# Optimization experiments

Measured on AMD Instinct MI355X. Metric: run time of the kernel, lower is better.

The kernel has to match this reference:

```python
import jax, jax.numpy as jnp
import numpy as np

TEMPERATURE = 0.5
EPS = 1e-12  # matches torch F.normalize eps


def _l2_normalize(x):
    norm = jnp.linalg.norm(x, axis=-1, keepdims=True)
    return x / jnp.maximum(norm, EPS)


def setup_inputs() -> dict:
    key = jax.random.key(0)
    k1, k2, k3 = jax.random.split(key, 3)
    N, D = 16384, 128
    self_predictions = jax.random.normal(k1, (N, D), dtype=jnp.float32)
    pos_predictions = jax.random.normal(k2, (N, D), dtype=jnp.float32)
    labels1 = jax.random.randint(k3, (N,), 0, 100, dtype=jnp.int64)
    return {
        "self_predictions": self_predictions,
        "pos_predictions": pos_predictions,
        "labels1": labels1,
    }


def reference(self_predictions, pos_predictions, labels1):
    N = labels1.shape[0]
    a = _l2_normalize(self_predictions)  # [N, D]
    b = _l2_normalize(pos_predictions)   # [N, D]
    # cosine similarity of already-normalized rows == dot product (GEMM form)
    sim = jnp.einsum("nd,md->nm", a, b)  # [N, N]
    neg_mask = (labels1[:, None] != labels1[None, :]).astype(sim.dtype)  # 1 - mask
    neg = jnp.exp(-sim / TEMPERATURE) * neg_mask
    return neg.sum() / (N * (N - 1))
```

## Files before the change

### kernel.cpp

```cpp
#include <hip/hip_runtime.h>

typedef unsigned char u8;
typedef unsigned short u16;
typedef float f32x4 __attribute__((ext_vector_type(4)));
typedef int i32x4 __attribute__((ext_vector_type(4)));
typedef int i32x8 __attribute__((ext_vector_type(8)));

#define NROWS 16384
#define DIM 128

#define NEG2LOG2E -2.8853900817779268f
#define SCALE ((float)(1.0 / (16384.0 * 16383.0)))

#define SCALE1 0x7F7F7F7F

#define KMAX 320

__global__ __launch_bounds__(256) void norm_kernel(
    const float* __restrict__ a, const float* __restrict__ b,
    u8* __restrict__ aO, u8* __restrict__ bO)
{
    int tid  = threadIdx.x;
    int lane = tid & 63;
    int w    = tid >> 6;
    int half = lane >> 5;
    int l32  = lane & 31;
    long row = (long)blockIdx.x * 8 + w * 2 + half;

    const float4 va = ((const float4*)(a + row * DIM))[l32];
    float sa = va.x * va.x + va.y * va.y + va.z * va.z + va.w * va.w;
    #pragma unroll
    for (int off = 16; off; off >>= 1) sa += __shfl_xor(sa, off, 64);
    float inva = 1.0f / fmaxf(sqrtf(sa), 1e-12f);
    int pa = __builtin_amdgcn_cvt_pk_fp8_f32(va.x * inva, va.y * inva, 0, false);
    pa = __builtin_amdgcn_cvt_pk_fp8_f32(va.z * inva, va.w * inva, pa, true);
    ((int*)(aO + row * DIM))[l32] = pa;

    const float4 vb = ((const float4*)(b + row * DIM))[l32];
    float sb = vb.x * vb.x + vb.y * vb.y + vb.z * vb.z + vb.w * vb.w;
    #pragma unroll
    for (int off = 16; off; off >>= 1) sb += __shfl_xor(sb, off, 64);
    float invb = NEG2LOG2E / fmaxf(sqrtf(sb), 1e-12f);
    int pb = __builtin_amdgcn_cvt_pk_fp8_f32(vb.x * invb, vb.y * invb, 0, false);
    pb = __builtin_amdgcn_cvt_pk_fp8_f32(vb.z * invb, vb.w * invb, pb, true);
    ((int*)(bO + row * DIM))[l32] = pb;
}

__global__ __launch_bounds__(256, 3) void gemm_kernel(
    const u8* __restrict__ A, const u8* __restrict__ B,
    const int* __restrict__ labels,
    float* __restrict__ partials, float* __restrict__ corrP)
{
    __shared__ u8 sA[16384];
    __shared__ u8 sB[2][16384];

    int tid  = threadIdx.x;
    int lane = tid & 63;
    int w    = tid >> 6;
    int mrow = lane & 15;
    int q    = lane >> 4;

    if (blockIdx.x == 32) {
        if (blockIdx.y >= 100) return;
        int l = blockIdx.y;
        int* sIdx = (int*)sA;
        __shared__ int sCnt;
        __shared__ float red[4];
        if (tid == 0) sCnt = 0;
        __syncthreads();

        for (int i = tid; i < NROWS; i += 256)
            if (labels[i] == l) {
                int p = atomicAdd(&sCnt, 1);
                if (p < KMAX) sIdx[p] = i;
            }
        __syncthreads();

        int k = sCnt < KMAX ? sCnt : KMAX;
        int nt = (k + 15) >> 4;
        int ntk = nt << 4;
        for (int r = k + tid; r < ntk; r += 256) sIdx[r] = sIdx[0];
        __syncthreads();

        float s = 0.0f;
        for (int tp = w; tp < nt * nt; tp += 4) {
            int ti = tp / nt, tj = tp - ti * nt;
            int ri = sIdx[ti * 16 + mrow];
            int rj = sIdx[tj * 16 + mrow];
            const u8* pa = A + (size_t)ri * DIM + q * 32;
            const u8* pb = B + (size_t)rj * DIM + q * 32;
            i32x8 aF, bF;
            *((i32x4*)&aF)     = *(const i32x4*)pa;
            *((i32x4*)&aF + 1) = *(const i32x4*)(pa + 16);
            *((i32x4*)&bF)     = *(const i32x4*)pb;
            *((i32x4*)&bF + 1) = *(const i32x4*)(pb + 16);
            f32x4 acc = (f32x4){0.f, 0.f, 0.f, 0.f};
            acc = __builtin_amdgcn_mfma_scale_f32_16x16x128_f8f6f4(
                aF, bF, acc, 0, 0, 0, SCALE1, 0, SCALE1);
            int i0 = ti * 16 + q * 4;
            int j  = tj * 16 + mrow;
            #pragma unroll
            for (int r = 0; r < 4; r++) {
                float e = __builtin_amdgcn_exp2f(acc[r]);
                s += ((i0 + r) < k && j < k) ? e : 0.0f;
            }
        }

        #pragma unroll
        for (int off = 32; off; off >>= 1) s += __shfl_xor(s, off, 64);
        if (lane == 0) red[w] = s;
        __syncthreads();
        if (tid == 0)
            corrP[l] = (red[0] + red[1] + red[2] + red[3]) * SCALE;
        return;
    }

    int wr = w >> 1;
    int wc = w & 1;

    int rowBase = blockIdx.y * 128;
    int colBase = blockIdx.x * 512;

    int m0 = tid >> 3;
    int p0 = tid & 7;
    int srcOff = m0 * 128 + ((p0 ^ (m0 & 7)) << 4);
    int ldsOff = (tid - lane) * 16;

    const u8* gA = A + (size_t)rowBase * DIM + srcOff;
    const u8* gB = B + (size_t)colBase * DIM + srcOff;

    {
        const u8* gpA = gA;
        const u8* gpB = gB;
        u8* lpA = &sA[ldsOff];
        u8* lpB = &sB[0][ldsOff];
        #pragma unroll
        for (int it = 0; it < 4; it++) {
            __builtin_amdgcn_global_load_lds(
                (const __attribute__((address_space(1))) void*)gpA,
                (__attribute__((address_space(3))) void*)lpA, 16, 0, 0);
            __builtin_amdgcn_global_load_lds(
                (const __attribute__((address_space(1))) void*)gpB,
                (__attribute__((address_space(3))) void*)lpB, 16, 0, 0);
            gpA += 4096; gpB += 4096; lpA += 4096; lpB += 4096;
        }
    }

    int aOff[4], bOff[4];
    #pragma unroll
    for (int mi = 0; mi < 4; mi++) {
        int m = wr * 64 + mi * 16 + mrow;
        aOff[mi] = m * 128 + (((q << 1) ^ (m & 7)) << 4);
        int n = wc * 64 + mi * 16 + mrow;
        bOff[mi] = n * 128 + (((q << 1) ^ (n & 7)) << 4);
    }

    __syncthreads();

    i32x8 a8[4];
    #pragma unroll
    for (int mi = 0; mi < 4; mi++) {
        *((i32x4*)&a8[mi])     = *(const i32x4*)(sA + aOff[mi]);
        *((i32x4*)&a8[mi] + 1) = *(const i32x4*)(sA + (aOff[mi] ^ 16));
    }

    float s = 0.0f;

    #pragma unroll
    for (int jt = 0; jt < 4; jt++) {
        if (jt < 3) {
            const u8* gp = gB + (jt + 1) * (128 * DIM);
            u8* lp = &sB[(jt + 1) & 1][ldsOff];
            #pragma unroll
            for (int it = 0; it < 4; it++) {
                __builtin_amdgcn_global_load_lds(
                    (const __attribute__((address_space(1))) void*)gp,
                    (__attribute__((address_space(3))) void*)lp, 16, 0, 0);
                gp += 4096; lp += 4096;
            }
        }

        const u8* sb = sB[jt & 1];
        i32x8 b8[4];
        #pragma unroll
        for (int ni = 0; ni < 4; ni++) {
            *((i32x4*)&b8[ni])     = *(const i32x4*)(sb + bOff[ni]);
            *((i32x4*)&b8[ni] + 1) = *(const i32x4*)(sb + (bOff[ni] ^ 16));
        }

        f32x4 acc[4][4];
        #pragma unroll
        for (int mi = 0; mi < 4; mi++)
            #pragma unroll
            for (int ni = 0; ni < 4; ni++)
                acc[mi][ni] = (f32x4){0.f, 0.f, 0.f, 0.f};

        #pragma unroll
        for (int mi = 0; mi < 4; mi++)
            #pragma unroll
            for (int ni = 0; ni < 4; ni++)
                acc[mi][ni] = __builtin_amdgcn_mfma_scale_f32_16x16x128_f8f6f4(
                    a8[mi], b8[ni], acc[mi][ni], 0, 0, 0, SCALE1, 0, SCALE1);

        float s0 = 0.0f, s1 = 0.0f;
        #pragma unroll
        for (int mi = 0; mi < 4; mi++)
            #pragma unroll
            for (int ni = 0; ni < 4; ni++)
                #pragma unroll
                for (int r = 0; r < 4; r++) {
                    float e = __builtin_amdgcn_exp2f(acc[mi][ni][r]);
                    if (r & 1) s1 += e; else s0 += e;
                }
        s += s0 + s1;

        __syncthreads();
    }

    #pragma unroll
    for (int off = 32; off; off >>= 1) s += __shfl_xor(s, off, 64);

    float* red = (float*)sA;
    if (lane == 0) red[w] = s;
    __syncthreads();
    if (tid == 0) {
        float t = (red[0] + red[1]) + (red[2] + red[3]);
        partials[blockIdx.y * 32 + blockIdx.x] = t * SCALE;
    }
}

__global__ __launch_bounds__(256) void reduce_kernel(
    const float* __restrict__ gP, const float* __restrict__ cP,
    float* __restrict__ out)
{
    int tid = threadIdx.x;
    const float4* p4 = (const float4*)gP;
    float s = 0.0f;
    #pragma unroll 4
    for (int i = tid; i < 1024; i += 256) {
        float4 v = p4[i];
        s += (v.x + v.y) + (v.z + v.w);
    }
    if (tid < 100) s -= cP[tid];
    #pragma unroll
    for (int off = 32; off; off >>= 1) s += __shfl_xor(s, off, 64);
    __shared__ float red[4];
    if ((tid & 63) == 0) red[tid >> 6] = s;
    __syncthreads();
    if (tid == 0) out[0] = (red[0] + red[1]) + (red[2] + red[3]);
}

extern "C" void kernel_launch(void* const* d_in, const int* in_sizes, int n_in,
                              void* d_out, int out_size, void* d_ws, size_t ws_size,
                              hipStream_t stream) {
    const float* self_p = (const float*)d_in[0];
    const float* pos_p  = (const float*)d_in[1];
    const int*   labels = (const int*)d_in[2];
    float* out = (float*)d_out;

    u8* aB = (u8*)d_ws;
    u8* bB = aB + (size_t)NROWS * DIM;
    float* gemmP = (float*)(bB + (size_t)NROWS * DIM);
    float* corrP = gemmP + 4096;

    norm_kernel<<<NROWS / 8, 256, 0, stream>>>(self_p, pos_p, aB, bB);
    gemm_kernel<<<dim3(33, 128), 256, 0, stream>>>(aB, bB, labels, gemmP, corrP);
    reduce_kernel<<<1, 256, 0, stream>>>(gemmP, corrP, out);
}
```

Measured before the change: 128.2 us.

## Flatten grid so correction blocks launch first, dual-issue MFMA tiles in correction

Switches the 2D grid to a 1D grid in which the 100 same-label correction blocks get the lowest block indices, so they are dispatched first rather than scattered across rows, and removes the 28 idle blocks. The correction loop now handles two tile pairs per iteration with two independent MFMAs and loads, to hide load latency. The intent is to keep the long correction blocks off the tail of the schedule. The cost is extra register pressure in the correction path.

```diff
diff --git a/kernel.cpp b/kernel.cpp
--- a/kernel.cpp
+++ b/kernel.cpp
@@ -15,6 +15,8 @@
 #define SCALE1 0x7F7F7F7F
 
 #define KMAX 320
+#define NCORR 100
+#define NGEMM 4096
 
 __global__ __launch_bounds__(256) void norm_kernel(
     const float* __restrict__ a, const float* __restrict__ b,
@@ -60,9 +62,8 @@
     int mrow = lane & 15;
     int q    = lane >> 4;
 
-    if (blockIdx.x == 32) {
-        if (blockIdx.y >= 100) return;
-        int l = blockIdx.y;
+    if (blockIdx.x < NCORR) {
+        int l = blockIdx.x;
         int* sIdx = (int*)sA;
         __shared__ int sCnt;
         __shared__ float red[4];
@@ -82,27 +83,48 @@
         for (int r = k + tid; r < ntk; r += 256) sIdx[r] = sIdx[0];
         __syncthreads();
 
+        int npairs = nt * nt;
         float s = 0.0f;
-        for (int tp = w; tp < nt * nt; tp += 4) {
-            int ti = tp / nt, tj = tp - ti * nt;
-            int ri = sIdx[ti * 16 + mrow];
-            int rj = sIdx[tj * 16 + mrow];
-            const u8* pa = A + (size_t)ri * DIM + q * 32;
-            const u8* pb = B + (size_t)rj * DIM + q * 32;
-            i32x8 aF, bF;
-            *((i32x4*)&aF)     = *(const i32x4*)pa;
-            *((i32x4*)&aF + 1) = *(const i32x4*)(pa + 16);
-            *((i32x4*)&bF)     = *(const i32x4*)pb;
-            *((i32x4*)&bF + 1) = *(const i32x4*)(pb + 16);
-            f32x4 acc = (f32x4){0.f, 0.f, 0.f, 0.f};
-            acc = __builtin_amdgcn_mfma_scale_f32_16x16x128_f8f6f4(
-                aF, bF, acc, 0, 0, 0, SCALE1, 0, SCALE1);
-            int i0 = ti * 16 + q * 4;
-            int j  = tj * 16 + mrow;
+        for (int tp = w; tp < npairs; tp += 8) {
+            int tpB = tp + 4;
+            bool has2 = tpB < npairs;
+            int tp2 = has2 ? tpB : tp;
+
+            int ti1 = tp / nt,  tj1 = tp  - ti1 * nt;
+            int ti2 = tp2 / nt, tj2 = tp2 - ti2 * nt;
+            int ri1 = sIdx[ti1 * 16 + mrow], rj1 = sIdx[tj1 * 16 + mrow];
+            int ri2 = sIdx[ti2 * 16 + mrow], rj2 = sIdx[tj2 * 16 + mrow];
+
+            const u8* pa1 = A + (size_t)ri1 * DIM + q * 32;
+            const u8* pb1 = B + (size_t)rj1 * DIM + q * 32;
+            const u8* pa2 = A + (size_t)ri2 * DIM + q * 32;
+            const u8* pb2 = B + (size_t)rj2 * DIM + q * 32;
+
+            i32x8 aF1, bF1, aF2, bF2;
+            *((i32x4*)&aF1)     = *(const i32x4*)pa1;
+            *((i32x4*)&aF1 + 1) = *(const i32x4*)(pa1 + 16);
+            *((i32x4*)&bF1)     = *(const i32x4*)pb1;
+            *((i32x4*)&bF1 + 1) = *(const i32x4*)(pb1 + 16);
+            *((i32x4*)&aF2)     = *(const i32x4*)pa2;
+            *((i32x4*)&aF2 + 1) = *(const i32x4*)(pa2 + 16);
+            *((i32x4*)&bF2)     = *(const i32x4*)pb2;
+            *((i32x4*)&bF2 + 1) = *(const i32x4*)(pb2 + 16);
+
+            f32x4 acc1 = (f32x4){0.f, 0.f, 0.f, 0.f};
+            f32x4 acc2 = (f32x4){0.f, 0.f, 0.f, 0.f};
+            acc1 = __builtin_amdgcn_mfma_scale_f32_16x16x128_f8f6f4(
+                aF1, bF1, acc1, 0, 0, 0, SCALE1, 0, SCALE1);
+            acc2 = __builtin_amdgcn_mfma_scale_f32_16x16x128_f8f6f4(
+                aF2, bF2, acc2, 0, 0, 0, SCALE1, 0, SCALE1);
+
+            int i1 = ti1 * 16 + q * 4, j1 = tj1 * 16 + mrow;
+            int i2 = ti2 * 16 + q * 4, j2 = tj2 * 16 + mrow;
             #pragma unroll
             for (int r = 0; r < 4; r++) {
-                float e = __builtin_amdgcn_exp2f(acc[r]);
-                s += ((i0 + r) < k && j < k) ? e : 0.0f;
+                float e1 = __builtin_amdgcn_exp2f(acc1[r]);
+                s += ((i1 + r) < k && j1 < k) ? e1 : 0.0f;
+                float e2 = __builtin_amdgcn_exp2f(acc2[r]);
+                s += (has2 && (i2 + r) < k && j2 < k) ? e2 : 0.0f;
             }
         }
 
@@ -115,11 +137,12 @@
         return;
     }
 
+    int g  = blockIdx.x - NCORR;
     int wr = w >> 1;
     int wc = w & 1;
 
-    int rowBase = blockIdx.y * 128;
-    int colBase = blockIdx.x * 512;
+    int rowBase = (g >> 5) * 128;
+    int colBase = (g & 31) * 512;
 
     int m0 = tid >> 3;
     int p0 = tid & 7;
@@ -225,7 +248,7 @@
     __syncthreads();
     if (tid == 0) {
         float t = (red[0] + red[1]) + (red[2] + red[3]);
-        partials[blockIdx.y * 32 + blockIdx.x] = t * SCALE;
+        partials[g] = t * SCALE;
     }
 }
 
@@ -241,7 +264,7 @@
         float4 v = p4[i];
         s += (v.x + v.y) + (v.z + v.w);
     }
-    if (tid < 100) s -= cP[tid];
+    if (tid < NCORR) s -= cP[tid];
     #pragma unroll
     for (int off = 32; off; off >>= 1) s += __shfl_xor(s, off, 64);
     __shared__ float red[4];
@@ -261,9 +284,9 @@
     u8* aB = (u8*)d_ws;
     u8* bB = aB + (size_t)NROWS * DIM;
     float* gemmP = (float*)(bB + (size_t)NROWS * DIM);
-    float* corrP = gemmP + 4096;
+    float* corrP = gemmP + NGEMM;
 
     norm_kernel<<<NROWS / 8, 256, 0, stream>>>(self_p, pos_p, aB, bB);
-    gemm_kernel<<<dim3(33, 128), 256, 0, stream>>>(aB, bB, labels, gemmP, corrP);
+    gemm_kernel<<<NCORR + NGEMM, 256, 0, stream>>>(aB, bB, labels, gemmP, corrP);
     reduce_kernel<<<1, 256, 0, stream>>>(gemmP, corrP, out);
 }
```

Result: faster. 112.7 us (-12.0%).

## Load A fragments from global, drop A LDS, split correction blocks into slices

Applied to the files above, without the earlier changes.

The GEMM kernel no longer stages the A tile in shared memory. Each wave loads its A fragments straight from global into registers, which cuts LDS use from 48KB to 32KB per block and may allow more resident blocks. The B swizzle is changed to a 256-byte, two-row pattern. The label-correction work is split into 8 slices per label (800 blocks) on a flat 1D grid, so a few long correction blocks no longer create a tail, and the reduce kernel now sums 800 correction partials. In exchange, the A fragment loads are uncoalesced and every block scans all labels 8 times.

```diff
diff --git a/kernel.cpp b/kernel.cpp
--- a/kernel.cpp
+++ b/kernel.cpp
@@ -1,7 +1,6 @@
 #include <hip/hip_runtime.h>
 
 typedef unsigned char u8;
-typedef unsigned short u16;
 typedef float f32x4 __attribute__((ext_vector_type(4)));
 typedef int i32x4 __attribute__((ext_vector_type(4)));
 typedef int i32x8 __attribute__((ext_vector_type(8)));
@@ -15,6 +14,8 @@
 #define SCALE1 0x7F7F7F7F
 
 #define KMAX 320
+#define NGEMM 4096
+#define NCORRB 800
 
 __global__ __launch_bounds__(256) void norm_kernel(
     const float* __restrict__ a, const float* __restrict__ b,
@@ -51,7 +52,6 @@
     const int* __restrict__ labels,
     float* __restrict__ partials, float* __restrict__ corrP)
 {
-    __shared__ u8 sA[16384];
     __shared__ u8 sB[2][16384];
 
     int tid  = threadIdx.x;
@@ -60,10 +60,10 @@
     int mrow = lane & 15;
     int q    = lane >> 4;
 
-    if (blockIdx.x == 32) {
-        if (blockIdx.y >= 100) return;
-        int l = blockIdx.y;
-        int* sIdx = (int*)sA;
+    if (blockIdx.x >= NGEMM) {
+        int b = blockIdx.x - NGEMM;
+        int l = b >> 3, slice = b & 7;
+        int* sIdx = (int*)sB;
         __shared__ int sCnt;
         __shared__ float red[4];
         if (tid == 0) sCnt = 0;
@@ -82,8 +82,9 @@
         for (int r = k + tid; r < ntk; r += 256) sIdx[r] = sIdx[0];
         __syncthreads();
 
+        int npairs = nt * nt;
         float s = 0.0f;
-        for (int tp = w; tp < nt * nt; tp += 4) {
+        for (int tp = slice * 4 + w; tp < npairs; tp += 32) {
             int ti = tp / nt, tj = tp - ti * nt;
             int ri = sIdx[ti * 16 + mrow];
             int rj = sIdx[tj * 16 + mrow];
@@ -111,58 +112,56 @@
         if (lane == 0) red[w] = s;
         __syncthreads();
         if (tid == 0)
-            corrP[l] = (red[0] + red[1] + red[2] + red[3]) * SCALE;
+            corrP[b] = (red[0] + red[1] + red[2] + red[3]) * SCALE;
         return;
     }
 
+    int g  = blockIdx.x;
     int wr = w >> 1;
     int wc = w & 1;
 
-    int rowBase = blockIdx.y * 128;
-    int colBase = blockIdx.x * 512;
-
-    int m0 = tid >> 3;
-    int p0 = tid & 7;
-    int srcOff = m0 * 128 + ((p0 ^ (m0 & 7)) << 4);
+    int rowBase = (g >> 5) * 128;
+    int colBase = (g & 31) * 512;
+
+    int S0 = tid >> 4;
+    int V  = (tid & 15) ^ (S0 & 15);
+    int srcOff = (S0 * 2 + (V >> 3)) * 128 + (V & 7) * 16;
     int ldsOff = (tid - lane) * 16;
 
-    const u8* gA = A + (size_t)rowBase * DIM + srcOff;
     const u8* gB = B + (size_t)colBase * DIM + srcOff;
 
     {
-        const u8* gpA = gA;
-        const u8* gpB = gB;
-        u8* lpA = &sA[ldsOff];
-        u8* lpB = &sB[0][ldsOff];
+        const u8* gp = gB;
+        u8* lp = &sB[0][ldsOff];
         #pragma unroll
         for (int it = 0; it < 4; it++) {
             __builtin_amdgcn_global_load_lds(
-                (const __attribute__((address_space(1))) void*)gpA,
-                (__attribute__((address_space(3))) void*)lpA, 16, 0, 0);
-            __builtin_amdgcn_global_load_lds(
-                (const __attribute__((address_space(1))) void*)gpB,
-                (__attribute__((address_space(3))) void*)lpB, 16, 0, 0);
-            gpA += 4096; gpB += 4096; lpA += 4096; lpB += 4096;
-        }
-    }
-
-    int aOff[4], bOff[4];
-    #pragma unroll
-    for (int mi = 0; mi < 4; mi++) {
-        int m = wr * 64 + mi * 16 + mrow;
-        aOff[mi] = m * 128 + (((q << 1) ^ (m & 7)) << 4);
-        int n = wc * 64 + mi * 16 + mrow;
-        bOff[mi] = n * 128 + (((q << 1) ^ (n & 7)) << 4);
+                (const __attribute__((address_space(1))) void*)gp,
+                (__attribute__((address_space(3))) void*)lp, 16, 0, 0);
+            gp += 4096; lp += 4096;
+        }
+    }
+
+    i32x8 a8[4];
+    {
+        const u8* gAf = A + (size_t)(rowBase + wr * 64 + mrow) * DIM + q * 32;
+        #pragma unroll
+        for (int mi = 0; mi < 4; mi++) {
+            const u8* p = gAf + mi * 16 * DIM;
+            *((i32x4*)&a8[mi])     = *(const i32x4*)p;
+            *((i32x4*)&a8[mi] + 1) = *(const i32x4*)(p + 16);
+        }
+    }
+
+    int bOff[4];
+    #pragma unroll
+    for (int ni = 0; ni < 4; ni++) {
+        int n = wc * 64 + ni * 16 + mrow;
+        int Vn = ((n & 1) << 3) | (q << 1);
+        bOff[ni] = (n >> 1) * 256 + ((Vn ^ ((n >> 1) & 15)) << 4);
     }
 
     __syncthreads();
-
-    i32x8 a8[4];
-    #pragma unroll
-    for (int mi = 0; mi < 4; mi++) {
-        *((i32x4*)&a8[mi])     = *(const i32x4*)(sA + aOff[mi]);
-        *((i32x4*)&a8[mi] + 1) = *(const i32x4*)(sA + (aOff[mi] ^ 16));
-    }
 
     float s = 0.0f;
 
@@ -220,12 +219,12 @@
     #pragma unroll
     for (int off = 32; off; off >>= 1) s += __shfl_xor(s, off, 64);
 
-    float* red = (float*)sA;
+    float* red = (float*)sB;
     if (lane == 0) red[w] = s;
     __syncthreads();
     if (tid == 0) {
         float t = (red[0] + red[1]) + (red[2] + red[3]);
-        partials[blockIdx.y * 32 + blockIdx.x] = t * SCALE;
+        partials[g] = t * SCALE;
     }
 }
 
@@ -241,7 +240,7 @@
         float4 v = p4[i];
         s += (v.x + v.y) + (v.z + v.w);
     }
-    if (tid < 100) s -= cP[tid];
+    for (int i = tid; i < NCORRB; i += 256) s -= cP[i];
     #pragma unroll
     for (int off = 32; off; off >>= 1) s += __shfl_xor(s, off, 64);
     __shared__ float red[4];
@@ -261,9 +260,9 @@
     u8* aB = (u8*)d_ws;
     u8* bB = aB + (size_t)NROWS * DIM;
     float* gemmP = (float*)(bB + (size_t)NROWS * DIM);
-    float* corrP = gemmP + 4096;
+    float* corrP = gemmP + NGEMM;
 
     norm_kernel<<<NROWS / 8, 256, 0, stream>>>(self_p, pos_p, aB, bB);
-    gemm_kernel<<<dim3(33, 128), 256, 0, stream>>>(aB, bB, labels, gemmP, corrP);
+    gemm_kernel<<<NGEMM + NCORRB, 256, 0, stream>>>(aB, bB, labels, gemmP, corrP);
     reduce_kernel<<<1, 256, 0, stream>>>(gemmP, corrP, out);
 }
```

After: 143.6 us. +12.0%, slower.
